# Optimization experiments

Hardware: AMD Instinct MI355X
Metric: run time of the kernel (lower is better)

The kernel has to match this reference:

```python
import jax, jax.numpy as jnp
import numpy as np

D_IN = 4096
D_OUT = 4096
RANK = 16
NUM_EXPERTS = 8
TOP_K = 2
SCALING = 32.0 / RANK  # lora_alpha / r = 2.0


def setup_inputs() -> dict:
    key = jax.random.key(0)
    ks = jax.random.split(key, 6)
    x = jax.random.normal(ks[0], (4, 2048, D_IN), dtype=jnp.float32)
    W_base = jax.random.normal(ks[1], (D_OUT, D_IN), dtype=jnp.float32) * (1.0 / np.sqrt(D_IN))
    b_base = jax.random.normal(ks[2], (D_OUT,), dtype=jnp.float32) * 0.01
    W_router = jax.random.normal(ks[3], (NUM_EXPERTS, D_IN), dtype=jnp.float32) * 0.01
    # kaiming-uniform-like A; B nonzero (module inits B to zero, but zero B makes outputs/grads trivial)
    A_stack = jax.random.uniform(ks[4], (NUM_EXPERTS, RANK, D_IN), dtype=jnp.float32,
                                 minval=-1.0, maxval=1.0) * (1.0 / np.sqrt(D_IN))
    B_stack = jax.random.normal(ks[5], (NUM_EXPERTS, D_OUT, RANK), dtype=jnp.float32) * 0.02
    return {"x": x, "W_base": W_base, "b_base": b_base,
            "W_router": W_router, "A_stack": A_stack, "B_stack": B_stack}


def reference(x, W_base, b_base, W_router, A_stack, B_stack):
    orig_shape = x.shape
    xf = x.reshape(-1, D_IN)                                # [N, d_in]
    # Router: softmax -> top-k -> renormalize
    logits = xf @ W_router.T                                # [N, E]
    probs = jax.nn.softmax(logits, axis=-1)
    topk_p, topk_i = jax.lax.top_k(probs, TOP_K)            # [N, K]
    topk_p = topk_p / jnp.sum(topk_p, axis=-1, keepdims=True)
    # Combine weights per expert (scatter top-k probs into [N, E])
    combine = jnp.sum(jax.nn.one_hot(topk_i, NUM_EXPERTS, dtype=xf.dtype)
                      * topk_p[..., None], axis=1)          # [N, E]
    # Low-rank expert path: x @ A_e^T, weight, then @ B_e^T, summed over experts
    h = jnp.einsum('nd,erd->ner', xf, A_stack)              # [N, E, r]
    h = h * combine[..., None]
    lora_out = jnp.einsum('ner,eor->no', h, B_stack) * SCALING  # [N, d_out]
    base_out = xf @ W_base.T + b_base                       # [N, d_out]
    out = base_out + lora_out
    return out.reshape(orig_shape[:-1] + (D_OUT,))
```

## Files before the change

### kernel.cpp

```cpp
#include <hip/hip_runtime.h>

#define D_IN   4096
#define D_OUT  4096
#define N_TOK  8192
#define RANK   16
#define NEXP   8
#define ER     128
#define KCAT   4224
#define SCALING 2.0f

typedef __attribute__((ext_vector_type(8))) short short8;
typedef __attribute__((ext_vector_type(4))) float f32x4;
typedef __attribute__((ext_vector_type(4))) unsigned short us4;
typedef unsigned int uint;

__device__ __forceinline__ unsigned short f2bf(float f) {
  unsigned u = __float_as_uint(f);
  u += 0x7FFFu + ((u >> 16) & 1u);
  return (unsigned short)(u >> 16);
}

__device__ __forceinline__ void gload_lds16(const void* g, void* l) {
  __builtin_amdgcn_global_load_lds(
      (const __attribute__((address_space(1))) unsigned int*)g,
      (__attribute__((address_space(3))) unsigned int*)l, 16, 0, 0);
}

__global__ __launch_bounds__(256) void fused_prep_router_kernel(
    const float* __restrict__ X, const float* __restrict__ Wr,
    const float* __restrict__ W, const float* __restrict__ A,
    const float* __restrict__ B,
    unsigned short* __restrict__ Xcat, float* __restrict__ Comb,
    unsigned short* __restrict__ Wcat, unsigned short* __restrict__ Ab) {
  if (blockIdx.x < 512) {
    int wave = threadIdx.x >> 6, lane = threadIdx.x & 63;
    int tok0 = blockIdx.x * 16 + wave * 4;
    float acc[4][8];
#pragma unroll
    for (int t = 0; t < 4; ++t)
#pragma unroll
      for (int e = 0; e < 8; ++e) acc[t][e] = 0.f;
    const float4* X4 = (const float4*)X;
    const float4* W4 = (const float4*)Wr;
#pragma unroll 1
    for (int it = 0; it < 16; ++it) {
      int kq = it * 64 + lane;
      float4 w[8];
#pragma unroll
      for (int e = 0; e < 8; ++e) w[e] = W4[e * 1024 + kq];
#pragma unroll
      for (int t = 0; t < 4; ++t) {
        float4 xv = X4[(size_t)(tok0 + t) * 1024 + kq];
        us4 xb = { f2bf(xv.x), f2bf(xv.y), f2bf(xv.z), f2bf(xv.w) };
        ((us4*)(Xcat + (size_t)(tok0 + t) * KCAT))[kq] = xb;
#pragma unroll
        for (int e = 0; e < 8; ++e)
          acc[t][e] = fmaf(xv.x, w[e].x, fmaf(xv.y, w[e].y,
                       fmaf(xv.z, w[e].z, fmaf(xv.w, w[e].w, acc[t][e]))));
      }
    }
#pragma unroll
    for (int t = 0; t < 4; ++t)
#pragma unroll
      for (int e = 0; e < 8; ++e) {
        float v = acc[t][e];
        for (int off = 32; off; off >>= 1) v += __shfl_xor(v, off, 64);
        acc[t][e] = v;
      }
#pragma unroll
    for (int t = 0; t < 4; ++t) {
      float m1 = acc[t][0]; int i1 = 0;
#pragma unroll
      for (int e = 1; e < 8; ++e) if (acc[t][e] > m1) { m1 = acc[t][e]; i1 = e; }
      float m2 = -1e30f; int i2 = 0;
#pragma unroll
      for (int e = 0; e < 8; ++e)
        if (e != i1 && acc[t][e] > m2) { m2 = acc[t][e]; i2 = e; }
      float w1 = 1.f / (1.f + expf(m2 - m1));
      if (lane < 8) {
        float v = (lane == i1) ? w1 : (lane == i2) ? (1.f - w1) : 0.f;
        Comb[(size_t)(tok0 + t) * 8 + lane] = v * SCALING;
      }
    }
  } else {
    const int NW4 = (D_OUT * D_IN) / 4;
    const int NA4 = (ER * D_IN) / 4;
    const int NB4 = (D_OUT * ER) / 4;
    const int total = NW4 + NA4 + NB4;
    const int stride = 2048 * 256;
    for (int i = (blockIdx.x - 512) * blockDim.x + threadIdx.x; i < total;
         i += stride) {
      if (i < NW4) {
        float4 v = ((const float4*)W)[i];
        us4 o = { f2bf(v.x), f2bf(v.y), f2bf(v.z), f2bf(v.w) };
        int row = i >> 10, kq = i & 1023;
        ((us4*)(Wcat + (size_t)row * KCAT))[kq] = o;
      } else if (i < NW4 + NA4) {
        int j = i - NW4;
        float4 v = ((const float4*)A)[j];
        us4 o = { f2bf(v.x), f2bf(v.y), f2bf(v.z), f2bf(v.w) };
        ((us4*)Ab)[j] = o;
      } else {
        int j = i - NW4 - NA4;
        int o = j >> 5; int rem = j & 31; int e = rem >> 2; int rq = rem & 3;
        float4 v = *(const float4*)(B + (size_t)e * D_OUT * RANK + o * RANK + rq * 4);
        us4 ob = { f2bf(v.x), f2bf(v.y), f2bf(v.z), f2bf(v.w) };
        *(us4*)(Wcat + (size_t)o * KCAT + D_IN + e * 16 + rq * 4) = ob;
      }
    }
  }
}

#define HSTG(S) { const uint hbase = (S) * 40960u; \
  _Pragma("unroll") for (int c = 0; c < 2; ++c) { gload_lds16(pa[c], ldsc + hbase + da[c]); pa[c] += 128; } \
  _Pragma("unroll") for (int c = 0; c < 8; ++c) { gload_lds16(pb[c], ldsc + hbase + db[c]); pb[c] += 128; } }

#define HTILE(S, S2, DOSTG, VM) { const uint hb = (S) * 40960u; \
  short8 af[4]; short8 bfr[4][4]; \
  _Pragma("unroll") for (int kk = 0; kk < 4; ++kk) af[kk] = *(const short8*)(ldsc + hb + oA[kk]); \
  _Pragma("unroll") for (int n = 0; n < 4; ++n) \
    _Pragma("unroll") for (int kk = 0; kk < 4; ++kk) bfr[n][kk] = *(const short8*)(ldsc + hb + oB[n][kk]); \
  if (DOSTG) HSTG(S2); \
  __builtin_amdgcn_sched_barrier(0); __builtin_amdgcn_s_barrier(); __builtin_amdgcn_sched_barrier(0); \
  __builtin_amdgcn_s_setprio(1); \
  _Pragma("unroll") for (int kk = 0; kk < 4; ++kk) \
    _Pragma("unroll") for (int n = 0; n < 4; ++n) \
      acc[n] = __builtin_amdgcn_mfma_f32_16x16x32_bf16(af[kk], bfr[n][kk], acc[n], 0, 0, 0); \
  __builtin_amdgcn_s_setprio(0); \
  __builtin_amdgcn_sched_barrier(0); \
  asm volatile("s_waitcnt vmcnt(" #VM ")" ::: ); \
  __builtin_amdgcn_s_barrier(); __builtin_amdgcn_sched_barrier(0); }

__global__ __launch_bounds__(256, 1) void h_gemm_kernel(
    unsigned short* Xcat, const unsigned short* __restrict__ Ab,
    const float* __restrict__ Comb) {
  __shared__ unsigned short hlds[61440];
  char* ldsc = (char*)hlds;
  const int tid = threadIdx.x, wave = tid >> 6, lane = tid & 63;
  const int wm = wave >> 1, wn = wave & 1;
  const int row0 = blockIdx.x * 32;

  const unsigned short* pa[2]; uint da[2];
#pragma unroll
  for (int c = 0; c < 2; ++c) {
    int ch = c * 256 + tid, row = ch >> 4, s = ch & 15;
    pa[c] = Xcat + (size_t)(row0 + row) * KCAT + (s ^ ((row >> 1) & 7)) * 8;
    da[c] = (uint)ch * 16;
  }
  const unsigned short* pb[8]; uint db[8];
#pragma unroll
  for (int c = 0; c < 8; ++c) {
    int ch = c * 256 + tid, row = ch >> 4, s = ch & 15;
    pb[c] = Ab + (size_t)row * D_IN + (s ^ ((row >> 1) & 7)) * 8;
    db[c] = 8192u + (uint)ch * 16;
  }

  uint oA[4], oB[4][4];
  {
    int rA = wm * 16 + (lane & 15);
#pragma unroll
    for (int kk = 0; kk < 4; ++kk) {
      int slot = kk * 4 + (lane >> 4);
      oA[kk] = (uint)rA * 256 + (uint)((slot ^ ((rA >> 1) & 7)) * 16);
    }
#pragma unroll
    for (int n = 0; n < 4; ++n) {
      int rB = wn * 64 + n * 16 + (lane & 15);
#pragma unroll
      for (int kk = 0; kk < 4; ++kk) {
        int slot = kk * 4 + (lane >> 4);
        oB[n][kk] = 8192u + (uint)rB * 256 + (uint)((slot ^ ((rB >> 1) & 7)) * 16);
      }
    }
  }

  f32x4 acc[4];
#pragma unroll
  for (int n = 0; n < 4; ++n) acc[n] = (f32x4){0.f, 0.f, 0.f, 0.f};

  HSTG(0); HSTG(1);
  asm volatile("s_waitcnt vmcnt(10)" ::: );
  __builtin_amdgcn_s_barrier();
  __builtin_amdgcn_sched_barrier(0);

#pragma unroll 1
  for (int i3 = 0; i3 < 10; ++i3) {
    HTILE(0, 2, 1, 10);
    HTILE(1, 0, 1, 10);
    HTILE(2, 1, 1, 10);
  }
  HTILE(0, 0, 0, 0);
  HTILE(1, 0, 0, 0);

#pragma unroll
  for (int n = 0; n < 4; ++n) {
    int c = wn * 64 + n * 16 + (lane & 15);
    int e = c >> 4;
#pragma unroll
    for (int i = 0; i < 4; ++i) {
      int r = row0 + wm * 16 + (lane >> 4) * 4 + i;
      float v = acc[n][i] * Comb[(size_t)r * 8 + e];
      Xcat[(size_t)r * KCAT + D_IN + c] = f2bf(v);
    }
  }
}

#define STG_A(S) { gload_lds16(pA0, ldsc + (S) * 32768u + dA0); pA0 += 32; \
                   gload_lds16(pA1, ldsc + (S) * 32768u + dA1); pA1 += 32; }
#define STG_B(S) { gload_lds16(pB0, ldsc + (S) * 32768u + dB0); pB0 += 32; \
                   gload_lds16(pB1, ldsc + (S) * 32768u + dB1); pB1 += 32; }

#define MT(SLOT, SLOT3, DOSTG, VMTOK, aCur, bCur, aNxt, bNxt, RDNEXT, LGTOK) { \
  const uint sb = (SLOT) * 32768u; \
  const uint sbn = (((SLOT) + 1) & 3) * 32768u; \
   \
  _Pragma("unroll") for (int m = 0; m < 4; ++m) \
    a1r[m] = *(const short8*)(ldsc + sb + offA[4 + m]); \
  if (DOSTG) STG_A(SLOT3); \
  __builtin_amdgcn_sched_barrier(0); \
  __builtin_amdgcn_s_barrier(); \
  __builtin_amdgcn_sched_barrier(0); \
  asm volatile("s_waitcnt lgkmcnt(4)" ::: ); \
  __builtin_amdgcn_sched_barrier(0); \
  __builtin_amdgcn_s_setprio(1); \
  _Pragma("unroll") for (int m = 0; m < 4; ++m) \
    _Pragma("unroll") for (int n = 0; n < 4; ++n) \
      acc[m][n] = __builtin_amdgcn_mfma_f32_16x16x32_bf16(aCur[m], bCur[n], acc[m][n], 0, 0, 0); \
  __builtin_amdgcn_s_setprio(0); \
  __builtin_amdgcn_sched_barrier(0); \
  asm volatile("s_waitcnt " VMTOK ::: ); \
  __builtin_amdgcn_s_barrier(); \
  __builtin_amdgcn_sched_barrier(0); \
   \
  if (RDNEXT) { \
    _Pragma("unroll") for (int m = 0; m < 4; ++m) \
      aNxt[m] = *(const short8*)(ldsc + sbn + offA[m]); \
    _Pragma("unroll") for (int n = 0; n < 4; ++n) \
      bNxt[n] = *(const short8*)(ldsc + sbn + offB[n]); \
  } \
  if (DOSTG) STG_B(SLOT3); \
  __builtin_amdgcn_sched_barrier(0); \
  __builtin_amdgcn_s_barrier(); \
  __builtin_amdgcn_sched_barrier(0); \
  asm volatile("s_waitcnt " LGTOK ::: ); \
  __builtin_amdgcn_sched_barrier(0); \
  __builtin_amdgcn_s_setprio(1); \
  _Pragma("unroll") for (int m = 0; m < 4; ++m) \
    _Pragma("unroll") for (int n = 0; n < 4; ++n) \
      acc[4 + m][n] = __builtin_amdgcn_mfma_f32_16x16x32_bf16(a1r[m], bCur[n], acc[4 + m][n], 0, 0, 0); \
  __builtin_amdgcn_s_setprio(0); \
  __builtin_amdgcn_sched_barrier(0); \
  __builtin_amdgcn_s_barrier(); \
  __builtin_amdgcn_sched_barrier(0); }

__global__ __launch_bounds__(512, 2) void main_gemm_kernel(
    const unsigned short* __restrict__ Xcat, const unsigned short* __restrict__ Wcat,
    const float* __restrict__ bias, float* __restrict__ Out) {
  __shared__ unsigned short lds[4 * 16384];
  char* ldsc = (char*)lds;
  const int tid = threadIdx.x;
  const int wave = tid >> 6, lane = tid & 63;
  const int wm = wave >> 2, wn = wave & 3;
  const int ks = lane >> 4;

  int bid = blockIdx.x;
  int swz = (bid & 7) * 64 + (bid >> 3);
  int mb = swz >> 4, nb = swz & 15;
  const int row0 = mb * 256, col0 = nb * 256;

  const unsigned short *pA0, *pA1, *pB0, *pB1;
  uint dA0, dA1, dB0, dB1;
  {
    int ch0 = tid, ch1 = 512 + tid;
    int rr0 = ch0 >> 2, ss0 = (ch0 & 3) ^ ((ch0 >> 3) & 3);
    int rr1 = ch1 >> 2, ss1 = (ch1 & 3) ^ ((ch1 >> 3) & 3);
    pA0 = Xcat + (size_t)(row0 + rr0) * KCAT + ss0 * 8;
    pA1 = Xcat + (size_t)(row0 + rr1) * KCAT + ss1 * 8;
    pB0 = Wcat + (size_t)(col0 + rr0) * KCAT + ss0 * 8;
    pB1 = Wcat + (size_t)(col0 + rr1) * KCAT + ss1 * 8;
    dA0 = (uint)wave * 1024;          dA1 = 8192u + (uint)wave * 1024;
    dB0 = 16384u + (uint)wave * 1024; dB1 = 24576u + (uint)wave * 1024;
  }

  uint offA[8], offB[4];
#pragma unroll
  for (int mi = 0; mi < 8; ++mi) {
    int r = wm * 128 + mi * 16 + (lane & 15);
    offA[mi] = (uint)r * 64 + (uint)((ks ^ ((r >> 1) & 3)) * 16);
  }
#pragma unroll
  for (int ni = 0; ni < 4; ++ni) {
    int r = wn * 64 + ni * 16 + (lane & 15);
    offB[ni] = 16384u + (uint)r * 64 + (uint)((ks ^ ((r >> 1) & 3)) * 16);
  }

  f32x4 acc[8][4];
#pragma unroll
  for (int mi = 0; mi < 8; ++mi)
#pragma unroll
    for (int ni = 0; ni < 4; ++ni) acc[mi][ni] = (f32x4){0.f, 0.f, 0.f, 0.f};

  short8 aAr[4], bAr[4], aBr[4], bBr[4], a1r[4];

  STG_A(0); STG_B(0); STG_A(1); STG_B(1); STG_A(2); STG_B(2);
  asm volatile("s_waitcnt vmcnt(8)" ::: );
  __builtin_amdgcn_s_barrier();
  __builtin_amdgcn_sched_barrier(0);
#pragma unroll
  for (int m = 0; m < 4; ++m) aAr[m] = *(const short8*)(ldsc + offA[m]);
#pragma unroll
  for (int n = 0; n < 4; ++n) bAr[n] = *(const short8*)(ldsc + offB[n]);
  __builtin_amdgcn_sched_barrier(0);

#pragma unroll 1
  for (int i4 = 0; i4 < 32; ++i4) {
    MT(0, 3, 1, "vmcnt(6)", aAr, bAr, aBr, bBr, 1, "lgkmcnt(8)");
    MT(1, 0, 1, "vmcnt(6)", aBr, bBr, aAr, bAr, 1, "lgkmcnt(8)");
    MT(2, 1, 1, "vmcnt(6)", aAr, bAr, aBr, bBr, 1, "lgkmcnt(8)");
    MT(3, 2, 1, "vmcnt(6)", aBr, bBr, aAr, bAr, 1, "lgkmcnt(8)");
  }
  MT(0, 3, 1, "vmcnt(6)", aAr, bAr, aBr, bBr, 1, "lgkmcnt(8)");
  MT(1, 0, 0, "vmcnt(4)", aBr, bBr, aAr, bAr, 1, "lgkmcnt(8)");
  MT(2, 0, 0, "vmcnt(0)", aAr, bAr, aBr, bBr, 1, "lgkmcnt(8)");
  MT(3, 0, 0, "vmcnt(0)", aBr, bBr, aAr, bAr, 0, "lgkmcnt(0)");

#pragma unroll
  for (int ni = 0; ni < 4; ++ni) {
    const int c = col0 + wn * 64 + ni * 16 + (lane & 15);
    const float bv = bias[c];
#pragma unroll
    for (int mi = 0; mi < 8; ++mi) {
#pragma unroll
      for (int i = 0; i < 4; ++i) {
        int r = row0 + wm * 128 + mi * 16 + ks * 4 + i;
        Out[(size_t)r * D_OUT + c] = acc[mi][ni][i] + bv;
      }
    }
  }
}

extern "C" void kernel_launch(void* const* d_in, const int* in_sizes, int n_in,
                              void* d_out, int out_size, void* d_ws, size_t ws_size,
                              hipStream_t stream) {
  const float* x        = (const float*)d_in[0];
  const float* W_base   = (const float*)d_in[1];
  const float* b_base   = (const float*)d_in[2];
  const float* W_router = (const float*)d_in[3];
  const float* A_stack  = (const float*)d_in[4];
  const float* B_stack  = (const float*)d_in[5];
  float* out = (float*)d_out;

  char* ws = (char*)d_ws;
  unsigned short* Xcat = (unsigned short*)(ws);
  unsigned short* Wcat = (unsigned short*)(ws + 69206016);
  unsigned short* Ab   = (unsigned short*)(ws + 103809024);
  float*          Comb = (float*)(ws + 104857600);

  hipLaunchKernelGGL(fused_prep_router_kernel, dim3(2560), dim3(256), 0, stream,
                     x, W_router, W_base, A_stack, B_stack, Xcat, Comb, Wcat, Ab);
  hipLaunchKernelGGL(h_gemm_kernel, dim3(256), dim3(256), 0, stream,
                     Xcat, Ab, Comb);
  hipLaunchKernelGGL(main_gemm_kernel, dim3(512), dim3(512), 0, stream,
                     Xcat, Wcat, b_base, out);
}
```

Before: 340.4 us.

## Restructure GEMM main loop to one barrier per k-tile with full-tile register prefetch

Replaces the two-half ping-pong macro (four barriers per k-tile, A split into two register halves) with a single-phase step. Each step prefetches all 8 A and 4 B fragments of the next LDS slot into the alternate register set, issues both global-to-LDS stages, runs all 32 MFMAs, then waits and synchronises once. This cuts barrier and waitcnt overhead per k-tile. In exchange it uses more VGPRs for the doubled fragment buffers, which risks spills under the 512x2 launch bounds, and LDS reads no longer overlap the MFMAs within a tile in the same way.

```diff
diff --git a/kernel.cpp b/kernel.cpp
--- a/kernel.cpp
+++ b/kernel.cpp
@@ -210,46 +210,26 @@
 #define STG_B(S) { gload_lds16(pB0, ldsc + (S) * 32768u + dB0); pB0 += 32; \
                    gload_lds16(pB1, ldsc + (S) * 32768u + dB1); pB1 += 32; }
 
-#define MT(SLOT, SLOT3, DOSTG, VMTOK, aCur, bCur, aNxt, bNxt, RDNEXT, LGTOK) { \
-  const uint sb = (SLOT) * 32768u; \
+#define MT2(SLOT, SLOT3, RD, STGON, VMTOK, aCur, bCur, aNxt, bNxt) { \
   const uint sbn = (((SLOT) + 1) & 3) * 32768u; \
-   \
-  _Pragma("unroll") for (int m = 0; m < 4; ++m) \
-    a1r[m] = *(const short8*)(ldsc + sb + offA[4 + m]); \
-  if (DOSTG) STG_A(SLOT3); \
-  __builtin_amdgcn_sched_barrier(0); \
-  __builtin_amdgcn_s_barrier(); \
-  __builtin_amdgcn_sched_barrier(0); \
-  asm volatile("s_waitcnt lgkmcnt(4)" ::: ); \
-  __builtin_amdgcn_sched_barrier(0); \
-  __builtin_amdgcn_s_setprio(1); \
-  _Pragma("unroll") for (int m = 0; m < 4; ++m) \
-    _Pragma("unroll") for (int n = 0; n < 4; ++n) \
-      acc[m][n] = __builtin_amdgcn_mfma_f32_16x16x32_bf16(aCur[m], bCur[n], acc[m][n], 0, 0, 0); \
-  __builtin_amdgcn_s_setprio(0); \
-  __builtin_amdgcn_sched_barrier(0); \
-  asm volatile("s_waitcnt " VMTOK ::: ); \
-  __builtin_amdgcn_s_barrier(); \
-  __builtin_amdgcn_sched_barrier(0); \
-   \
-  if (RDNEXT) { \
-    _Pragma("unroll") for (int m = 0; m < 4; ++m) \
+  if (RD) { \
+    _Pragma("unroll") for (int m = 0; m < 8; ++m) \
       aNxt[m] = *(const short8*)(ldsc + sbn + offA[m]); \
     _Pragma("unroll") for (int n = 0; n < 4; ++n) \
       bNxt[n] = *(const short8*)(ldsc + sbn + offB[n]); \
   } \
-  if (DOSTG) STG_B(SLOT3); \
-  __builtin_amdgcn_sched_barrier(0); \
-  __builtin_amdgcn_s_barrier(); \
-  __builtin_amdgcn_sched_barrier(0); \
-  asm volatile("s_waitcnt " LGTOK ::: ); \
+  __builtin_amdgcn_sched_barrier(0); \
+  if (STGON) { STG_A(SLOT3); STG_B(SLOT3); } \
   __builtin_amdgcn_sched_barrier(0); \
   __builtin_amdgcn_s_setprio(1); \
-  _Pragma("unroll") for (int m = 0; m < 4; ++m) \
+  _Pragma("unroll") for (int m = 0; m < 8; ++m) \
     _Pragma("unroll") for (int n = 0; n < 4; ++n) \
-      acc[4 + m][n] = __builtin_amdgcn_mfma_f32_16x16x32_bf16(a1r[m], bCur[n], acc[4 + m][n], 0, 0, 0); \
+      acc[m][n] = __builtin_amdgcn_mfma_f32_16x16x32_bf16(aCur[m], bCur[n], acc[m][n], 0, 0, 0); \
   __builtin_amdgcn_s_setprio(0); \
   __builtin_amdgcn_sched_barrier(0); \
+  asm volatile("s_waitcnt lgkmcnt(0)" ::: ); \
+  __builtin_amdgcn_sched_barrier(0); \
+  asm volatile("s_waitcnt " VMTOK ::: ); \
   __builtin_amdgcn_s_barrier(); \
   __builtin_amdgcn_sched_barrier(0); }
 
@@ -300,29 +280,30 @@
 #pragma unroll
     for (int ni = 0; ni < 4; ++ni) acc[mi][ni] = (f32x4){0.f, 0.f, 0.f, 0.f};
 
-  short8 aAr[4], bAr[4], aBr[4], bBr[4], a1r[4];
+  short8 aE[8], bE[4], aO[8], bO[4];
 
   STG_A(0); STG_B(0); STG_A(1); STG_B(1); STG_A(2); STG_B(2);
-  asm volatile("s_waitcnt vmcnt(8)" ::: );
+  asm volatile("s_waitcnt vmcnt(4)" ::: );
   __builtin_amdgcn_s_barrier();
   __builtin_amdgcn_sched_barrier(0);
 #pragma unroll
-  for (int m = 0; m < 4; ++m) aAr[m] = *(const short8*)(ldsc + offA[m]);
-#pragma unroll
-  for (int n = 0; n < 4; ++n) bAr[n] = *(const short8*)(ldsc + offB[n]);
+  for (int m = 0; m < 8; ++m) aE[m] = *(const short8*)(ldsc + offA[m]);
+#pragma unroll
+  for (int n = 0; n < 4; ++n) bE[n] = *(const short8*)(ldsc + offB[n]);
+  asm volatile("s_waitcnt lgkmcnt(0)" ::: );
   __builtin_amdgcn_sched_barrier(0);
 
 #pragma unroll 1
   for (int i4 = 0; i4 < 32; ++i4) {
-    MT(0, 3, 1, "vmcnt(6)", aAr, bAr, aBr, bBr, 1, "lgkmcnt(8)");
-    MT(1, 0, 1, "vmcnt(6)", aBr, bBr, aAr, bAr, 1, "lgkmcnt(8)");
-    MT(2, 1, 1, "vmcnt(6)", aAr, bAr, aBr, bBr, 1, "lgkmcnt(8)");
-    MT(3, 2, 1, "vmcnt(6)", aBr, bBr, aAr, bAr, 1, "lgkmcnt(8)");
-  }
-  MT(0, 3, 1, "vmcnt(6)", aAr, bAr, aBr, bBr, 1, "lgkmcnt(8)");
-  MT(1, 0, 0, "vmcnt(4)", aBr, bBr, aAr, bAr, 1, "lgkmcnt(8)");
-  MT(2, 0, 0, "vmcnt(0)", aAr, bAr, aBr, bBr, 1, "lgkmcnt(8)");
-  MT(3, 0, 0, "vmcnt(0)", aBr, bBr, aAr, bAr, 0, "lgkmcnt(0)");
+    MT2(0, 3, 1, 1, "vmcnt(4)", aE, bE, aO, bO);
+    MT2(1, 0, 1, 1, "vmcnt(4)", aO, bO, aE, bE);
+    MT2(2, 1, 1, 1, "vmcnt(4)", aE, bE, aO, bO);
+    MT2(3, 2, 1, 1, "vmcnt(4)", aO, bO, aE, bE);
+  }
+  MT2(0, 3, 1, 1, "vmcnt(4)", aE, bE, aO, bO);
+  MT2(1, 0, 1, 0, "vmcnt(0)", aO, bO, aE, bE);
+  MT2(2, 0, 1, 0, "vmcnt(0)", aE, bE, aO, bO);
+  MT2(3, 0, 0, 0, "vmcnt(0)", aO, bO, aE, bE);
 
 #pragma unroll
   for (int ni = 0; ni < 4; ++ni) {
```

Result: slower. 368.0 us (+8.1%).
